# Optimization experiments

Measured on AMD Instinct MI355X. Metric: run time of the kernel, lower is better.

The kernel has to match this reference:

```python
import jax, jax.numpy as jnp
import numpy as np
import math

B, L, N, DIM, H = 2, 8, 1024, 512, 8
DH = DIM // H

def setup_inputs() -> dict:
    key = jax.random.key(0)
    ks = jax.random.split(key, 9)
    s = 1.0 / math.sqrt(DIM)
    return {
        "x": jax.random.normal(ks[0], (B, L, N, DIM), dtype=jnp.float32),
        "Wq": jax.random.normal(ks[1], (DIM, DIM), dtype=jnp.float32) * s,
        "bq": jnp.zeros((DIM,), dtype=jnp.float32),
        "Wk": jax.random.normal(ks[2], (DIM, DIM), dtype=jnp.float32) * s,
        "bk": jnp.zeros((DIM,), dtype=jnp.float32),
        "Wv": jax.random.normal(ks[3], (DIM, DIM), dtype=jnp.float32) * s,
        "bv": jnp.zeros((DIM,), dtype=jnp.float32),
        "Wo": jax.random.normal(ks[4], (DIM, DIM), dtype=jnp.float32) * s,
        "bo": jnp.zeros((DIM,), dtype=jnp.float32),
    }

def _split_heads(t):
    # 'b l n (h d) -> b l h n d'
    b, l, n, _ = t.shape
    return t.reshape(b, l, n, H, DH).transpose(0, 1, 3, 2, 4)

def reference(x, Wq, bq, Wk, bk, Wv, bv, Wo, bo):
    q = _split_heads(x @ Wq.T + bq)
    # FAITHFUL BUG: source maps (q, v, k) -> (q_mat, k_mat, v_mat),
    # so the "keys" come from the v projection and "values" from the k projection.
    k_mat = _split_heads(x @ Wv.T + bv)
    v_mat = _split_heads(x @ Wk.T + bk)
    # scale is sqrt(Dh * num_heads) = sqrt(dim), as in the source
    scores = jnp.einsum('blhnd,blhmd->blhnm', q, k_mat) / math.sqrt(DIM)
    weights = jax.nn.softmax(scores, axis=-1)
    inter = jnp.einsum('blhnm,blhmd->blhnd', weights, v_mat)
    # 'b l h n d -> b l n (h d)'
    inter = inter.transpose(0, 1, 3, 2, 4).reshape(x.shape[0], x.shape[1], x.shape[2], DIM)
    return inter @ Wo.T + bo
```

## Files before the change

kernel.cpp:

```cpp
#include <hip/hip_runtime.h>
#include <stdint.h>

#define DIMC 512
#define NSEQ 1024
#define BLT  16
#define NHEAD 8
#define DHD  64
#define MTOT (BLT*NSEQ)

typedef float f32x4 __attribute__((ext_vector_type(4)));
typedef short s16x8 __attribute__((ext_vector_type(8)));
typedef short s16x4 __attribute__((ext_vector_type(4)));

__device__ __forceinline__ unsigned short f2bf(float f) {
    unsigned int u = __float_as_uint(f);
    u += 0x7fffu + ((u >> 16) & 1u);
    return (unsigned short)(u >> 16);
}
__device__ __forceinline__ float bf2f(unsigned short h) {
    return __uint_as_float(((unsigned int)h) << 16);
}

#define QSCALE (0.04419417382415922f * 1.4426950408889634f)

__device__ __forceinline__ void gll16(const void* g, void* l) {
    __builtin_amdgcn_global_load_lds(
        (const __attribute__((address_space(1))) void*)g,
        (__attribute__((address_space(3))) void*)l, 16, 0, 0);
}

__device__ __forceinline__ f32x4 mfma16_bf16(s16x4 a, s16x4 b, f32x4 c) {
#if __has_builtin(__builtin_amdgcn_mfma_f32_16x16x16bf16_1k)
    return __builtin_amdgcn_mfma_f32_16x16x16bf16_1k(a, b, c, 0, 0, 0);
#else
    asm volatile("v_mfma_f32_16x16x16_bf16 %0, %1, %2, %0"
                 : "+v"(c) : "v"(a), "v"(b));
    return c;
#endif
}

__device__ __forceinline__ bool detect_bf16(const unsigned short* x) {
    int t = threadIdx.x & 63;
    unsigned short v = x[2 * t];
    int e = (v >> 7) & 0xFF;
    unsigned long long ball = __ballot(e < 100 || e > 137);
    return __popcll(ball) < 16;
}

struct ConvArgs {
    const void* src[9];
    unsigned short* dst[9];
};

__global__ __launch_bounds__(256) void conv_kernel(ConvArgs a,
                                                   const unsigned short* __restrict__ xdet) {
    const bool isbf = detect_bf16(xdet);
    int b = blockIdx.x;
    int seg, idx;
    if (b < 4096)      { seg = 0; idx = (b * 256 + threadIdx.x) * 8; }
    else if (b < 4608) { int t = b - 4096; seg = 1 + (t >> 7);
                         idx = (((t & 127) * 256) + threadIdx.x) * 8; }
    else               { int i = threadIdx.x * 8; seg = 5 + (i >> 9); idx = i & 511; }
    const void* s = a.src[seg];
    unsigned short* d = a.dst[seg];
    if (isbf) {
        *(uint4*)(d + idx) = *(const uint4*)((const unsigned short*)s + idx);
    } else {
        float4 t0 = *(const float4*)((const float*)s + idx);
        float4 t1 = *(const float4*)((const float*)s + idx + 4);
        ushort4 v0{f2bf(t0.x), f2bf(t0.y), f2bf(t0.z), f2bf(t0.w)};
        ushort4 v1{f2bf(t1.x), f2bf(t1.y), f2bf(t1.z), f2bf(t1.w)};
        *(ushort4*)(d + idx)     = v0;
        *(ushort4*)(d + idx + 4) = v1;
    }
}

__device__ __forceinline__ void gemm_core_async(
    const unsigned short* __restrict__ Ap, const unsigned short* __restrict__ Wp,
    int mBase, int nBase, unsigned short* Al, unsigned short* Bl, f32x4 acc[4][4])
{
    const int wave = threadIdx.x >> 6;
    const int lane = threadIdx.x & 63;
    const int lr = lane & 15, lg = lane >> 4;
    const int wm = wave >> 1, wn = wave & 1;
    const int srow = lane >> 3;
    const int scol = (lane & 7) * 8;

    #pragma unroll
    for (int a = 0; a < 4; ++a)
        #pragma unroll
        for (int b = 0; b < 4; ++b) acc[a][b] = (f32x4){0.f, 0.f, 0.f, 0.f};

    for (int k0 = 0; k0 < DIMC; k0 += 64) {
        #pragma unroll
        for (int i = 0; i < 4; ++i) {
            int rbase = (wave * 4 + i) * 8;
            gll16(Ap + (long)(mBase + rbase + srow) * DIMC + k0 + scol, Al + rbase * 64);
            gll16(Wp + (long)(nBase + rbase + srow) * DIMC + k0 + scol, Bl + rbase * 64);
        }
        __syncthreads();

        #pragma unroll
        for (int kk = 0; kk < 64; kk += 32) {
            s16x8 af[4], bf_[4];
            #pragma unroll
            for (int a = 0; a < 4; ++a)
                af[a] = *(const s16x8*)&Al[(wm * 64 + a * 16 + lr) * 64 + kk + lg * 8];
            #pragma unroll
            for (int b = 0; b < 4; ++b)
                bf_[b] = *(const s16x8*)&Bl[(wn * 64 + b * 16 + lr) * 64 + kk + lg * 8];
            #pragma unroll
            for (int a = 0; a < 4; ++a)
                #pragma unroll
                for (int b = 0; b < 4; ++b)
                    acc[a][b] = __builtin_amdgcn_mfma_f32_16x16x32_bf16(af[a], bf_[b], acc[a][b], 0, 0, 0);
        }
        __syncthreads();
    }
}

__global__ __launch_bounds__(256) void proj_kernel(
    const unsigned short* __restrict__ xb,
    const unsigned short* __restrict__ Wqb, const unsigned short* __restrict__ Wkb,
    const unsigned short* __restrict__ Wvb,
    const unsigned short* __restrict__ bqb, const unsigned short* __restrict__ bkb,
    const unsigned short* __restrict__ bvb,
    unsigned short* __restrict__ Q, unsigned short* __restrict__ K,
    unsigned short* __restrict__ Vt)
{
    const int z = blockIdx.z;
    const unsigned short* Wp = (z == 0) ? Wqb : ((z == 1) ? Wvb : Wkb);
    const unsigned short* bp = (z == 0) ? bqb : ((z == 1) ? bvb : bkb);
    unsigned short* outp = (z == 0) ? Q : ((z == 1) ? K : Vt);
    const float oscale = (z == 0) ? QSCALE : 1.0f;

    const int mBase = blockIdx.x * 128;
    const int nBase = blockIdx.y * 128;
    const int lane = threadIdx.x & 63;
    const int lr = lane & 15, lg = lane >> 4;
    const int wm = (threadIdx.x >> 6) >> 1, wn = (threadIdx.x >> 6) & 1;

    __shared__ unsigned short Al[128 * 64];
    __shared__ unsigned short Bl[128 * 64];
    f32x4 acc[4][4];
    gemm_core_async(xb, Wp, mBase, nBase, Al, Bl, acc);

    #pragma unroll
    for (int b = 0; b < 4; ++b) {
        int j = nBase + wn * 64 + b * 16 + lr;
        float bb = bf2f(bp[j]);
        int h = j >> 6, d = j & 63;
        #pragma unroll
        for (int a = 0; a < 4; ++a) {
            int m0 = mBase + wm * 64 + a * 16 + lg * 4;
            int bl = m0 >> 10, n0 = m0 & 1023;
            if (z == 2) {
                ushort4 pk;
                unsigned short* p = (unsigned short*)&pk;
                #pragma unroll
                for (int r = 0; r < 4; ++r) p[r] = f2bf(acc[a][b][r] + bb);
                *(ushort4*)&outp[(((bl << 3) + h) << 16) + (d << 10) + n0] = pk;
            } else {
                #pragma unroll
                for (int r = 0; r < 4; ++r) {
                    float v = (acc[a][b][r] + bb) * oscale;
                    outp[(((bl << 3) + h) << 16) + ((n0 + r) << 6) + d] = f2bf(v);
                }
            }
        }
    }
}

__global__ __launch_bounds__(256) void out_gemm_kernel(
    const unsigned short* __restrict__ inter, const unsigned short* __restrict__ Wob,
    const unsigned short* __restrict__ bob, void* __restrict__ outp,
    const unsigned short* __restrict__ xdet)
{
    const bool isbf = detect_bf16(xdet);
    const int mBase = blockIdx.x * 128;
    const int nBase = blockIdx.y * 128;
    const int lane = threadIdx.x & 63;
    const int lr = lane & 15, lg = lane >> 4;
    const int wm = (threadIdx.x >> 6) >> 1, wn = (threadIdx.x >> 6) & 1;

    __shared__ unsigned short Al[128 * 64];
    __shared__ unsigned short Bl[128 * 64];
    f32x4 acc[4][4];
    gemm_core_async(inter, Wob, mBase, nBase, Al, Bl, acc);

    #pragma unroll
    for (int b = 0; b < 4; ++b) {
        int j = nBase + wn * 64 + b * 16 + lr;
        float bb = bf2f(bob[j]);
        #pragma unroll
        for (int a = 0; a < 4; ++a) {
            #pragma unroll
            for (int r = 0; r < 4; ++r) {
                long m = mBase + wm * 64 + a * 16 + lg * 4 + r;
                float v = acc[a][b][r] + bb;
                if (isbf) ((unsigned short*)outp)[m * DIMC + j] = f2bf(v);
                else      ((float*)outp)[m * DIMC + j] = v;
            }
        }
    }
}

#define SWZ(row, col) ((row) * 64 + ((col) ^ (((row) & 7) * 8)))

__global__ __launch_bounds__(256, 3) void attn_kernel(
    const unsigned short* __restrict__ Q, const unsigned short* __restrict__ K,
    const unsigned short* __restrict__ Vt, unsigned short* __restrict__ inter)
{
    const int b = blockIdx.x;
    const int bh = b & 127;
    const int qt = b >> 7;
    const int wave = threadIdx.x >> 6;
    const int lane = threadIdx.x & 63;
    const int lr = lane & 15;
    const int lg = lane >> 4;

    const unsigned short* Qb = Q + (long)bh * (NSEQ * DHD);
    const int qbase = qt * 128 + wave * 32;

    s16x8 qf[2][2];
    #pragma unroll
    for (int g = 0; g < 2; ++g)
        #pragma unroll
        for (int kk = 0; kk < 2; ++kk)
            qf[g][kk] = *(const s16x8*)&Qb[(qbase + g * 16 + lr) * DHD + kk * 32 + lg * 8];

    __shared__ unsigned short Kl[64 * 64];
    __shared__ unsigned short Vl[64 * 64];

    f32x4 o[2][4];
    #pragma unroll
    for (int g = 0; g < 2; ++g)
        #pragma unroll
        for (int m = 0; m < 4; ++m) o[g][m] = (f32x4){0.f, 0.f, 0.f, 0.f};
    float l_acc[2] = {0.f, 0.f};

    for (int kt = 0; kt < 16; ++kt) {
        const unsigned short* Kb = K + (long)bh * (NSEQ * DHD) + kt * 64 * DHD;
        const unsigned short* Vb = Vt + (long)bh * (NSEQ * DHD) + kt * 64;

        #pragma unroll
        for (int i = 0; i < 2; ++i) {
            int f = threadIdx.x + 256 * i;
            int row = f >> 3, c8 = (f & 7) * 8;
            *(uint4*)&Kl[SWZ(row, c8)] = *(const uint4*)&Kb[row * DHD + c8];
            *(uint4*)&Vl[SWZ(row, c8)] = *(const uint4*)&Vb[row * NSEQ + c8];
        }
        __syncthreads();

        f32x4 s[2][4];
        #pragma unroll
        for (int g = 0; g < 2; ++g)
            #pragma unroll
            for (int c = 0; c < 4; ++c) s[g][c] = (f32x4){0.f, 0.f, 0.f, 0.f};
        #pragma unroll
        for (int kk = 0; kk < 2; ++kk) {
            s16x8 af[4];
            #pragma unroll
            for (int c = 0; c < 4; ++c)
                af[c] = *(const s16x8*)&Kl[SWZ(c * 16 + lr, kk * 32 + lg * 8)];
            #pragma unroll
            for (int g = 0; g < 2; ++g)
                #pragma unroll
                for (int c = 0; c < 4; ++c)
                    s[g][c] = __builtin_amdgcn_mfma_f32_16x16x32_bf16(af[c], qf[g][kk], s[g][c], 0, 0, 0);
        }

        s16x4 pb[2][4];
        #pragma unroll
        for (int g = 0; g < 2; ++g)
            #pragma unroll
            for (int c = 0; c < 4; ++c) {
                float p0 = __builtin_exp2f(s[g][c][0]);
                float p1 = __builtin_exp2f(s[g][c][1]);
                float p2 = __builtin_exp2f(s[g][c][2]);
                float p3 = __builtin_exp2f(s[g][c][3]);
                l_acc[g] += (p0 + p1) + (p2 + p3);
                unsigned int u0 = __float_as_uint(p0) + 0x8000u;
                unsigned int u1 = __float_as_uint(p1) + 0x8000u;
                unsigned int u2 = __float_as_uint(p2) + 0x8000u;
                unsigned int u3 = __float_as_uint(p3) + 0x8000u;
                union { s16x4 v; unsigned int u[2]; } pk;
                pk.u[0] = __builtin_amdgcn_perm(u1, u0, 0x07060302u);
                pk.u[1] = __builtin_amdgcn_perm(u3, u2, 0x07060302u);
                pb[g][c] = pk.v;
            }

        #pragma unroll
        for (int c = 0; c < 4; ++c) {
            s16x4 va[4];
            #pragma unroll
            for (int m = 0; m < 4; ++m)
                va[m] = *(const s16x4*)&Vl[SWZ(m * 16 + lr, c * 16 + lg * 4)];
            #pragma unroll
            for (int g = 0; g < 2; ++g)
                #pragma unroll
                for (int m = 0; m < 4; ++m)
                    o[g][m] = mfma16_bf16(va[m], pb[g][c], o[g][m]);
        }
        __syncthreads();
    }

    const int bl = bh >> 3, h = bh & 7;
    #pragma unroll
    for (int g = 0; g < 2; ++g) {
        float l = l_acc[g];
        l += __shfl_xor(l, 16);
        l += __shfl_xor(l, 32);
        float inv = 1.f / l;
        const int n = qbase + g * 16 + lr;
        #pragma unroll
        for (int m = 0; m < 4; ++m) {
            ushort4 pk;
            unsigned short* p = (unsigned short*)&pk;
            #pragma unroll
            for (int r = 0; r < 4; ++r) p[r] = f2bf(o[g][m][r] * inv);
            *(ushort4*)&inter[((long)(bl * NSEQ + n)) * DIMC + h * 64 + m * 16 + lg * 4] = pk;
        }
    }
}

extern "C" void kernel_launch(void* const* d_in, const int* in_sizes, int n_in,
                              void* d_out, int out_size, void* d_ws, size_t ws_size,
                              hipStream_t stream) {
    const void* x  = d_in[0];
    const void* Wq = d_in[1]; const void* bq = d_in[2];
    const void* Wk = d_in[3]; const void* bk = d_in[4];
    const void* Wv = d_in[5]; const void* bv = d_in[6];
    const void* Wo = d_in[7]; const void* bo = d_in[8];

    char* ws = (char*)d_ws;
    unsigned short* xb  = (unsigned short*)ws;
    unsigned short* Q   = xb + (long)MTOT * DIMC;
    unsigned short* K   = Q  + (long)MTOT * DIMC;
    unsigned short* Vt  = K  + (long)MTOT * DIMC;
    unsigned short* Wqb = Vt + (long)MTOT * DIMC;
    unsigned short* Wkb = Wqb + DIMC * DIMC;
    unsigned short* Wvb = Wkb + DIMC * DIMC;
    unsigned short* Wob = Wvb + DIMC * DIMC;
    unsigned short* bqb = Wob + DIMC * DIMC;
    unsigned short* bkb = bqb + DIMC;
    unsigned short* bvb = bkb + DIMC;
    unsigned short* bob = bvb + DIMC;

    ConvArgs ca;
    ca.src[0] = x;  ca.src[1] = Wq; ca.src[2] = Wk; ca.src[3] = Wv; ca.src[4] = Wo;
    ca.src[5] = bq; ca.src[6] = bk; ca.src[7] = bv; ca.src[8] = bo;
    ca.dst[0] = xb;  ca.dst[1] = Wqb; ca.dst[2] = Wkb; ca.dst[3] = Wvb; ca.dst[4] = Wob;
    ca.dst[5] = bqb; ca.dst[6] = bkb; ca.dst[7] = bvb; ca.dst[8] = bob;
    conv_kernel<<<4609, 256, 0, stream>>>(ca, (const unsigned short*)x);

    dim3 gp(MTOT / 128, DIMC / 128, 3);
    proj_kernel<<<gp, 256, 0, stream>>>(xb, Wqb, Wkb, Wvb, bqb, bkb, bvb, Q, K, Vt);

    attn_kernel<<<8 * 128, 256, 0, stream>>>(Q, K, Vt, xb );

    dim3 go(MTOT / 128, DIMC / 128);
    out_gemm_kernel<<<go, 256, 0, stream>>>(xb , Wob, bob, d_out,
                                            (const unsigned short*)x);
}
```

Baseline: 224.7 us.

## Double-buffer K/V tiles via async LDS loads and compute row sums with MFMA

The attention loop now stages K and V tiles into two LDS buffers using global_load_lds, prefetching the next tile while the current one is computed. This removes one barrier per iteration and hides global load latency behind compute. It also replaces the manual bf16 rounding with v_cvt_pk_bf16_f32, moves the softmax denominator accumulation onto MFMA against a ones vector (which drops the final shuffles), and raises wave priority around MFMA blocks. The costs are doubled LDS use, which may reduce occupancy, and a denominator summed from bf16-rounded probabilities.

```diff
diff --git a/kernel.cpp b/kernel.cpp
--- a/kernel.cpp
+++ b/kernel.cpp
@@ -37,6 +37,13 @@
                  : "+v"(c) : "v"(a), "v"(b));
     return c;
 #endif
+}
+
+__device__ __forceinline__ s16x4 pack_bf16x4(float p0, float p1, float p2, float p3) {
+    union { unsigned int u[2]; s16x4 v; } pk;
+    asm("v_cvt_pk_bf16_f32 %0, %1, %2" : "=v"(pk.u[0]) : "v"(p0), "v"(p1));
+    asm("v_cvt_pk_bf16_f32 %0, %1, %2" : "=v"(pk.u[1]) : "v"(p2), "v"(p3));
+    return pk.v;
 }
 
 __device__ __forceinline__ bool detect_bf16(const unsigned short* x) {
@@ -214,8 +221,9 @@
     const int b = blockIdx.x;
     const int bh = b & 127;
     const int qt = b >> 7;
-    const int wave = threadIdx.x >> 6;
-    const int lane = threadIdx.x & 63;
+    const int tid = threadIdx.x;
+    const int wave = tid >> 6;
+    const int lane = tid & 63;
     const int lr = lane & 15;
     const int lg = lane >> 4;
 
@@ -229,28 +237,44 @@
         for (int kk = 0; kk < 2; ++kk)
             qf[g][kk] = *(const s16x8*)&Qb[(qbase + g * 16 + lr) * DHD + kk * 32 + lg * 8];
 
-    __shared__ unsigned short Kl[64 * 64];
-    __shared__ unsigned short Vl[64 * 64];
+    __shared__ unsigned short Kl[2][64 * 64];
+    __shared__ unsigned short Vl[2][64 * 64];
+
+    const int srow = tid >> 3;
+    const int scol = ((tid & 7) * 8) ^ ((srow & 7) * 8);
+    const unsigned short* kp = K  + (long)bh * (NSEQ * DHD) + srow * DHD  + scol;
+    const unsigned short* vp = Vt + (long)bh * (NSEQ * DHD) + srow * NSEQ + scol;
+
+    auto stage = [&](int buf, long ko, long vo) {
+        unsigned short* Kb_ = &Kl[buf][0];
+        unsigned short* Vb_ = &Vl[buf][0];
+        gll16(kp + ko,         Kb_ + wave * 512);
+        gll16(kp + ko + 2048,  Kb_ + wave * 512 + 2048);
+        gll16(vp + vo,         Vb_ + wave * 512);
+        gll16(vp + vo + 32768, Vb_ + wave * 512 + 2048);
+    };
 
     f32x4 o[2][4];
-    #pragma unroll
-    for (int g = 0; g < 2; ++g)
+    f32x4 lacc[2];
+    #pragma unroll
+    for (int g = 0; g < 2; ++g) {
+        lacc[g] = (f32x4){0.f, 0.f, 0.f, 0.f};
         #pragma unroll
         for (int m = 0; m < 4; ++m) o[g][m] = (f32x4){0.f, 0.f, 0.f, 0.f};
-    float l_acc[2] = {0.f, 0.f};
-
+    }
+    const s16x4 onesf = {(short)0x3F80, (short)0x3F80, (short)0x3F80, (short)0x3F80};
+
+    stage(0, 0, 0);
+    __syncthreads();
+
+    #pragma unroll 2
     for (int kt = 0; kt < 16; ++kt) {
-        const unsigned short* Kb = K + (long)bh * (NSEQ * DHD) + kt * 64 * DHD;
-        const unsigned short* Vb = Vt + (long)bh * (NSEQ * DHD) + kt * 64;
-
-        #pragma unroll
-        for (int i = 0; i < 2; ++i) {
-            int f = threadIdx.x + 256 * i;
-            int row = f >> 3, c8 = (f & 7) * 8;
-            *(uint4*)&Kl[SWZ(row, c8)] = *(const uint4*)&Kb[row * DHD + c8];
-            *(uint4*)&Vl[SWZ(row, c8)] = *(const uint4*)&Vb[row * NSEQ + c8];
-        }
-        __syncthreads();
+        const int cur = kt & 1;
+        if (kt < 15)
+            stage(cur ^ 1, (long)(kt + 1) * (64 * DHD), (long)(kt + 1) * 64);
+
+        const unsigned short* Kc = &Kl[cur][0];
+        const unsigned short* Vc = &Vl[cur][0];
 
         f32x4 s[2][4];
         #pragma unroll
@@ -262,56 +286,49 @@
             s16x8 af[4];
             #pragma unroll
             for (int c = 0; c < 4; ++c)
-                af[c] = *(const s16x8*)&Kl[SWZ(c * 16 + lr, kk * 32 + lg * 8)];
+                af[c] = *(const s16x8*)&Kc[SWZ(c * 16 + lr, kk * 32 + lg * 8)];
+            __builtin_amdgcn_s_setprio(1);
             #pragma unroll
             for (int g = 0; g < 2; ++g)
                 #pragma unroll
                 for (int c = 0; c < 4; ++c)
                     s[g][c] = __builtin_amdgcn_mfma_f32_16x16x32_bf16(af[c], qf[g][kk], s[g][c], 0, 0, 0);
-        }
-
-        s16x4 pb[2][4];
-        #pragma unroll
-        for (int g = 0; g < 2; ++g)
-            #pragma unroll
-            for (int c = 0; c < 4; ++c) {
+            __builtin_amdgcn_s_setprio(0);
+        }
+
+        #pragma unroll
+        for (int c = 0; c < 4; ++c) {
+            s16x4 pb[2];
+            #pragma unroll
+            for (int g = 0; g < 2; ++g) {
                 float p0 = __builtin_exp2f(s[g][c][0]);
                 float p1 = __builtin_exp2f(s[g][c][1]);
                 float p2 = __builtin_exp2f(s[g][c][2]);
                 float p3 = __builtin_exp2f(s[g][c][3]);
-                l_acc[g] += (p0 + p1) + (p2 + p3);
-                unsigned int u0 = __float_as_uint(p0) + 0x8000u;
-                unsigned int u1 = __float_as_uint(p1) + 0x8000u;
-                unsigned int u2 = __float_as_uint(p2) + 0x8000u;
-                unsigned int u3 = __float_as_uint(p3) + 0x8000u;
-                union { s16x4 v; unsigned int u[2]; } pk;
-                pk.u[0] = __builtin_amdgcn_perm(u1, u0, 0x07060302u);
-                pk.u[1] = __builtin_amdgcn_perm(u3, u2, 0x07060302u);
-                pb[g][c] = pk.v;
+                pb[g] = pack_bf16x4(p0, p1, p2, p3);
             }
-
-        #pragma unroll
-        for (int c = 0; c < 4; ++c) {
             s16x4 va[4];
             #pragma unroll
             for (int m = 0; m < 4; ++m)
-                va[m] = *(const s16x4*)&Vl[SWZ(m * 16 + lr, c * 16 + lg * 4)];
-            #pragma unroll
-            for (int g = 0; g < 2; ++g)
+                va[m] = *(const s16x4*)&Vc[SWZ(m * 16 + lr, c * 16 + lg * 4)];
+            __builtin_amdgcn_s_setprio(1);
+            #pragma unroll
+            for (int g = 0; g < 2; ++g) {
+                lacc[g] = mfma16_bf16(onesf, pb[g], lacc[g]);
                 #pragma unroll
                 for (int m = 0; m < 4; ++m)
-                    o[g][m] = mfma16_bf16(va[m], pb[g][c], o[g][m]);
-        }
-        __syncthreads();
+                    o[g][m] = mfma16_bf16(va[m], pb[g], o[g][m]);
+            }
+            __builtin_amdgcn_s_setprio(0);
+        }
+
+        if (kt < 15) __syncthreads();
     }
 
     const int bl = bh >> 3, h = bh & 7;
     #pragma unroll
     for (int g = 0; g < 2; ++g) {
-        float l = l_acc[g];
-        l += __shfl_xor(l, 16);
-        l += __shfl_xor(l, 32);
-        float inv = 1.f / l;
+        float inv = 1.f / lacc[g][0];
         const int n = qbase + g * 16 + lr;
         #pragma unroll
         for (int m = 0; m < 4; ++m) {
```

Measured after the change: 218.2 us. 1.03x faster.
